# Kernel optimization log

Measured on AMD Instinct MI355X. Metric: run time of the kernel, lower is better.

## Reference

```python
import jax, jax.numpy as jnp
import numpy as np

N_WIRES = 4
N_LAYERS = 3


def _ry_batched(theta):
    # theta: (N,) -> (N,2,2) complex64 RY matrices
    c = jnp.cos(theta / 2).astype(jnp.complex64)
    s = jnp.sin(theta / 2).astype(jnp.complex64)
    row0 = jnp.stack([c, -s], axis=-1)
    row1 = jnp.stack([s, c], axis=-1)
    return jnp.stack([row0, row1], axis=-2)


def _rot(phi, theta, omega):
    # PennyLane Rot(phi,theta,omega) = RZ(omega) @ RY(theta) @ RZ(phi), 2x2 complex
    c = jnp.cos(theta / 2)
    s = jnp.sin(theta / 2)
    m00 = jnp.exp(-0.5j * (phi + omega)) * c
    m01 = -jnp.exp(0.5j * (phi - omega)) * s
    m10 = jnp.exp(-0.5j * (phi - omega)) * s
    m11 = jnp.exp(0.5j * (phi + omega)) * c
    return jnp.stack([jnp.stack([m00, m01]), jnp.stack([m10, m11])]).astype(jnp.complex64)


def _apply_1q(state, U, wire):
    # state: (N,2,2,2,2); U: (2,2) shared or (N,2,2) per-state
    s = jnp.moveaxis(state, wire + 1, 1)
    if U.ndim == 2:
        s = jnp.einsum('ij,njklm->niklm', U, s)
    else:
        s = jnp.einsum('nij,njklm->niklm', U, s)
    return jnp.moveaxis(s, 1, wire + 1)


def _cnot(state, ctrl, tgt):
    # flip target axis where control axis == 1
    s = jnp.moveaxis(state, (ctrl + 1, tgt + 1), (1, 2))
    s = jnp.stack([s[:, 0], jnp.flip(s[:, 1], axis=1)], axis=1)
    return jnp.moveaxis(s, (1, 2), (ctrl + 1, tgt + 1))


def _circuit(angles, params):
    # angles: (N,4) encoding rotations; params: (L,4,3) StronglyEntanglingLayers weights
    N = angles.shape[0]
    state = jnp.zeros((N, 2, 2, 2, 2), jnp.complex64).at[:, 0, 0, 0, 0].set(1.0)
    for w in range(N_WIRES):
        state = _apply_1q(state, _ry_batched(angles[:, w]), w)
    for l in range(params.shape[0]):
        for w in range(N_WIRES):
            state = _apply_1q(state, _rot(params[l, w, 0], params[l, w, 1], params[l, w, 2]), w)
        r = (l % (N_WIRES - 1)) + 1  # PennyLane default ranges
        for w in range(N_WIRES):
            state = _cnot(state, w, (w + r) % N_WIRES)
    probs = state.real ** 2 + state.imag ** 2  # (N,2,2,2,2)
    z = jnp.array([1.0, -1.0], jnp.float32)
    exps = []
    for w in range(N_WIRES):
        axes = tuple(a for a in range(1, 5) if a != w + 1)
        exps.append(probs.sum(axes) @ z)  # <Z_w>
    return jnp.stack(exps, axis=-1)  # (N,4)


def setup_inputs() -> dict:
    key = jax.random.key(0)
    k1, k2, k3, k4 = jax.random.split(key, 4)
    B = 4096
    x = jax.random.uniform(k1, (B, 1, 28, 28), dtype=jnp.float32)
    ansatz_params = jax.random.normal(k2, (N_LAYERS, N_WIRES, 3), dtype=jnp.float32)
    lim = 1.0 / np.sqrt(4.0)
    W = jax.random.uniform(k3, (4, 4), dtype=jnp.float32, minval=-lim, maxval=lim)
    b = jax.random.uniform(k4, (4,), dtype=jnp.float32, minval=-lim, maxval=lim)
    return {'x': x, 'ansatz_params': ansatz_params, 'W': W, 'b': b}


def reference(x, ansatz_params, W, b):
    B = x.shape[0]
    img = x.reshape(B, 28, 28)
    # 2x2 non-overlapping patches, row-major within patch: (B,14,14,2,2)->(B*196,4)
    patches = img.reshape(B, 14, 2, 14, 2).transpose(0, 1, 3, 2, 4).reshape(B * 196, 4)
    feats = _circuit(patches, ansatz_params)  # (B*196,4)
    out = feats @ W.T + b  # per-patch linear
    return out.reshape(B, 196 * 4)
```

## Files before the change

### kernel.cpp

```cpp
#include <hip/hip_runtime.h>
#include <math.h>

#define NW 4
#define NL 3

struct cplx { float re, im; };
__device__ __forceinline__ cplx cmul(cplx a, cplx b){ return {a.re*b.re - a.im*b.im, a.re*b.im + a.im*b.re}; }
__device__ __forceinline__ cplx cadd(cplx a, cplx b){ return {a.re+b.re, a.im+b.im}; }

__global__ void precompute_T(const float* __restrict__ params,
                             const float* __restrict__ W,
                             const float* __restrict__ bias,
                             float* __restrict__ ws)
{
    __shared__ float Ure[16][16], Uim[16][16];
    __shared__ float C[4][16][16];
    const int tid = threadIdx.x;
    const int s = tid >> 4, c = tid & 15;

    Ure[s][c] = (s == c) ? 1.f : 0.f;
    Uim[s][c] = 0.f;
    __syncthreads();

    for (int l = 0; l < NL; ++l) {
        for (int w = 0; w < NW; ++w) {
            float phi = params[(l*NW + w)*3 + 0];
            float th  = params[(l*NW + w)*3 + 1];
            float om  = params[(l*NW + w)*3 + 2];
            float st, ct; sincosf(0.5f*th, &st, &ct);
            float sp, cp; sincosf(-0.5f*(phi+om), &sp, &cp);
            float sm, cm; sincosf(-0.5f*(phi-om), &sm, &cm);
            cplx m00 = {  cp*ct,  sp*ct };
            cplx m01 = { -cm*st,  sm*st };
            cplx m10 = {  cm*st,  sm*st };
            cplx m11 = {  cp*ct, -sp*ct };
            int mask = 1 << (3 - w);
            int b = (s & mask) ? 1 : 0;
            int s0 = s & ~mask, s1 = s | mask;
            cplx g0 = b ? m10 : m00;
            cplx g1 = b ? m11 : m01;
            cplx u0 = { Ure[s0][c], Uim[s0][c] };
            cplx u1 = { Ure[s1][c], Uim[s1][c] };
            cplx nv = cadd(cmul(g0,u0), cmul(g1,u1));
            __syncthreads();
            Ure[s][c] = nv.re; Uim[s][c] = nv.im;
            __syncthreads();
        }
        int r = (l % (NW-1)) + 1;
        for (int w = 0; w < NW; ++w) {
            int ctrl = w, tgt = (w + r) % NW;
            int cmk = 1 << (3 - ctrl), tmk = 1 << (3 - tgt);
            int src = (s & cmk) ? (s ^ tmk) : s;
            float vr = Ure[src][c], vi = Uim[src][c];
            __syncthreads();
            Ure[s][c] = vr; Uim[s][c] = vi;
            __syncthreads();
        }
    }

    {
        float A[4];
        for (int w = 0; w < NW; ++w) {
            int mask = 1 << (3 - w);
            float acc = 0.f;
            for (int rr = 0; rr < 16; ++rr) {
                float zs = (rr & mask) ? -1.f : 1.f;
                acc += zs * (Ure[rr][s]*Ure[rr][c] + Uim[rr][s]*Uim[rr][c]);
            }
            A[w] = acc;
        }
        for (int j = 0; j < 4; ++j) {
            float cj = 0.f;
            for (int w = 0; w < NW; ++w) cj += W[j*4 + w] * A[w];
            C[j][s][c] = cj;
        }
    }
    __syncthreads();

    if (tid < 81) {
        int k = tid;
        int kw[4] = { k/27, (k/9)%3, (k/3)%3, k%3 };
        int sb[4][2], tb[4][2]; float sg[4][2];
        for (int w = 0; w < 4; ++w) {
            int kk = kw[w];
            if (kk == 0)      { sb[w][0]=0; tb[w][0]=0; sg[w][0]= 1.f; sb[w][1]=1; tb[w][1]=1; sg[w][1]= 1.f; }
            else if (kk == 1) { sb[w][0]=0; tb[w][0]=0; sg[w][0]= 1.f; sb[w][1]=1; tb[w][1]=1; sg[w][1]=-1.f; }
            else              { sb[w][0]=0; tb[w][0]=1; sg[w][0]= 1.f; sb[w][1]=1; tb[w][1]=0; sg[w][1]= 1.f; }
        }
        float acc[4] = {0.f,0.f,0.f,0.f};
        for (int m = 0; m < 16; ++m) {
            int ss = 0, tt = 0; float sign = 1.f;
            for (int w = 0; w < 4; ++w) {
                int o = (m >> (3-w)) & 1;
                ss |= sb[w][o] << (3-w);
                tt |= tb[w][o] << (3-w);
                sign *= sg[w][o];
            }
            for (int j = 0; j < 4; ++j) acc[j] += sign * C[j][ss][tt];
        }
        for (int j = 0; j < 4; ++j) {
            float v = acc[j] * (1.f/16.f);
            if (k == 0) v += bias[j];
            ws[k*4 + j] = v;
        }
    }
}

__device__ __forceinline__ void build9(float a0, float a1, float* p) {
    float c0, s0, c1, s1;
    __sincosf(a0, &s0, &c0);
    __sincosf(a1, &s1, &c1);
    p[0] = 1.f;  p[1] = c1;    p[2] = s1;
    p[3] = c0;   p[4] = c0*c1; p[5] = c0*s1;
    p[6] = s0;   p[7] = s0*c1; p[8] = s0*s1;
}

__global__ __launch_bounds__(256) void quanv_main(const float* __restrict__ x,
                                                  const float* __restrict__ T,
                                                  float* __restrict__ out)
{
    __shared__ float4 sT[81];
    const int tid = threadIdx.x;
    if (tid < 81) sT[tid] = ((const float4*)T)[tid];
    __syncthreads();

    int t   = blockIdx.x * 256 + tid;
    int jt  = t % 7;
    int rem = t / 7;
    int i   = rem % 14;
    int b   = rem / 14;

    const float* base = x + b*784 + (2*i)*28 + 4*jt;
    float4 r0 = *(const float4*)(base);
    float4 r1 = *(const float4*)(base + 28);

    float pA01[9], pA23[9], pB01[9], pB23[9];
    build9(r0.x, r0.y, pA01);  build9(r1.x, r1.y, pA23);
    build9(r0.z, r0.w, pB01);  build9(r1.z, r1.w, pB23);

    float oA0=0.f,oA1=0.f,oA2=0.f,oA3=0.f;
    float oB0=0.f,oB1=0.f,oB2=0.f,oB3=0.f;
    #pragma unroll
    for (int u = 0; u < 9; ++u) {
        float au = pA01[u], bu = pB01[u];
        #pragma unroll
        for (int v = 0; v < 9; ++v) {
            float4 tv = sT[u*9 + v];
            float qA = au * pA23[v];
            float qB = bu * pB23[v];
            oA0 = fmaf(tv.x, qA, oA0);  oB0 = fmaf(tv.x, qB, oB0);
            oA1 = fmaf(tv.y, qA, oA1);  oB1 = fmaf(tv.y, qB, oB1);
            oA2 = fmaf(tv.z, qA, oA2);  oB2 = fmaf(tv.z, qB, oB2);
            oA3 = fmaf(tv.w, qA, oA3);  oB3 = fmaf(tv.w, qB, oB3);
        }
    }

    int p = b*196 + i*14 + 2*jt;
    float4* o = (float4*)out + p;
    o[0] = make_float4(oA0, oA1, oA2, oA3);
    o[1] = make_float4(oB0, oB1, oB2, oB3);
}

extern "C" void kernel_launch(void* const* d_in, const int* in_sizes, int n_in,
                              void* d_out, int out_size, void* d_ws, size_t ws_size,
                              hipStream_t stream) {
    const float* x      = (const float*)d_in[0];
    const float* params = (const float*)d_in[1];
    const float* W      = (const float*)d_in[2];
    const float* bias   = (const float*)d_in[3];
    float* out = (float*)d_out;
    float* ws  = (float*)d_ws;

    precompute_T<<<1, 256, 0, stream>>>(params, W, bias, ws);

    const int total  = 4096 * 14 * 7;
    const int blocks = total / 256;
    quanv_main<<<blocks, 256, 0, stream>>>(x, ws, out);
}
```

Before: 84.71 us.

## Process four patches per thread and move unitary build into registers

The main kernel now has each thread handle a 2x2 group of patches (four patches) instead of two. Each shared-memory read of the transfer table is reused across four accumulators, and the block size drops to 64 threads. The precompute kernel builds the 16x16 circuit unitary column by column in registers on 16 threads, replacing the sync-heavy shared-memory gate loop, and computes the gate matrices once. The main risk is higher register pressure and fewer threads in flight in the main kernel.

```diff
diff --git a/kernel.cpp b/kernel.cpp
--- a/kernel.cpp
+++ b/kernel.cpp
@@ -3,75 +3,92 @@
 
 #define NW 4
 #define NL 3
-
-struct cplx { float re, im; };
-__device__ __forceinline__ cplx cmul(cplx a, cplx b){ return {a.re*b.re - a.im*b.im, a.re*b.im + a.im*b.re}; }
-__device__ __forceinline__ cplx cadd(cplx a, cplx b){ return {a.re+b.re, a.im+b.im}; }
 
 __global__ void precompute_T(const float* __restrict__ params,
                              const float* __restrict__ W,
                              const float* __restrict__ bias,
                              float* __restrict__ ws)
 {
+    __shared__ float4 gm4[12][2];
     __shared__ float Ure[16][16], Uim[16][16];
     __shared__ float C[4][16][16];
     const int tid = threadIdx.x;
-    const int s = tid >> 4, c = tid & 15;
-
-    Ure[s][c] = (s == c) ? 1.f : 0.f;
-    Uim[s][c] = 0.f;
-    __syncthreads();
-
-    for (int l = 0; l < NL; ++l) {
-        for (int w = 0; w < NW; ++w) {
-            float phi = params[(l*NW + w)*3 + 0];
-            float th  = params[(l*NW + w)*3 + 1];
-            float om  = params[(l*NW + w)*3 + 2];
-            float st, ct; sincosf(0.5f*th, &st, &ct);
-            float sp, cp; sincosf(-0.5f*(phi+om), &sp, &cp);
-            float sm, cm; sincosf(-0.5f*(phi-om), &sm, &cm);
-            cplx m00 = {  cp*ct,  sp*ct };
-            cplx m01 = { -cm*st,  sm*st };
-            cplx m10 = {  cm*st,  sm*st };
-            cplx m11 = {  cp*ct, -sp*ct };
-            int mask = 1 << (3 - w);
-            int b = (s & mask) ? 1 : 0;
-            int s0 = s & ~mask, s1 = s | mask;
-            cplx g0 = b ? m10 : m00;
-            cplx g1 = b ? m11 : m01;
-            cplx u0 = { Ure[s0][c], Uim[s0][c] };
-            cplx u1 = { Ure[s1][c], Uim[s1][c] };
-            cplx nv = cadd(cmul(g0,u0), cmul(g1,u1));
-            __syncthreads();
-            Ure[s][c] = nv.re; Uim[s][c] = nv.im;
-            __syncthreads();
-        }
-        int r = (l % (NW-1)) + 1;
-        for (int w = 0; w < NW; ++w) {
-            int ctrl = w, tgt = (w + r) % NW;
-            int cmk = 1 << (3 - ctrl), tmk = 1 << (3 - tgt);
-            int src = (s & cmk) ? (s ^ tmk) : s;
-            float vr = Ure[src][c], vi = Uim[src][c];
-            __syncthreads();
-            Ure[s][c] = vr; Uim[s][c] = vi;
-            __syncthreads();
-        }
-    }
+
+    if (tid < 12) {
+        float phi = params[tid*3 + 0];
+        float th  = params[tid*3 + 1];
+        float om  = params[tid*3 + 2];
+        float st, ct; sincosf(0.5f*th, &st, &ct);
+        float sp, cp; sincosf(-0.5f*(phi+om), &sp, &cp);
+        float sm, cm; sincosf(-0.5f*(phi-om), &sm, &cm);
+        gm4[tid][0] = make_float4( cp*ct,  sp*ct, -cm*st,  sm*st);
+        gm4[tid][1] = make_float4( cm*st,  sm*st,  cp*ct, -sp*ct);
+    }
+    __syncthreads();
+
+    if (tid < 16) {
+        const int col = tid;
+        float ur[16], ui[16];
+        #pragma unroll
+        for (int r = 0; r < 16; ++r) { ur[r] = (r == col) ? 1.f : 0.f; ui[r] = 0.f; }
+
+        #pragma unroll
+        for (int l = 0; l < NL; ++l) {
+            #pragma unroll
+            for (int w = 0; w < NW; ++w) {
+                float4 g0 = gm4[l*4 + w][0];
+                float4 g1 = gm4[l*4 + w][1];
+                const int mask = 1 << (3 - w);
+                #pragma unroll
+                for (int s = 0; s < 16; ++s) {
+                    if (s & mask) continue;
+                    const int s1 = s | mask;
+                    float u0r = ur[s],  u0i = ui[s];
+                    float u1r = ur[s1], u1i = ui[s1];
+                    ur[s]  = (g0.x*u0r - g0.y*u0i) + (g0.z*u1r - g0.w*u1i);
+                    ui[s]  = (g0.x*u0i + g0.y*u0r) + (g0.z*u1i + g0.w*u1r);
+                    ur[s1] = (g1.x*u0r - g1.y*u0i) + (g1.z*u1r - g1.w*u1i);
+                    ui[s1] = (g1.x*u0i + g1.y*u0r) + (g1.z*u1i + g1.w*u1r);
+                }
+            }
+            const int rr = (l % (NW-1)) + 1;
+            #pragma unroll
+            for (int w = 0; w < NW; ++w) {
+                const int cmk = 1 << (3 - w);
+                const int tmk = 1 << (3 - ((w + rr) % NW));
+                #pragma unroll
+                for (int s = 0; s < 16; ++s) {
+                    if ((s & cmk) && !(s & tmk)) {
+                        const int s1 = s | tmk;
+                        float tr = ur[s], ti = ui[s];
+                        ur[s] = ur[s1]; ui[s] = ui[s1];
+                        ur[s1] = tr;    ui[s1] = ti;
+                    }
+                }
+            }
+        }
+        #pragma unroll
+        for (int r = 0; r < 16; ++r) { Ure[r][col] = ur[r]; Uim[r][col] = ui[r]; }
+    }
+    __syncthreads();
 
     {
-        float A[4];
-        for (int w = 0; w < NW; ++w) {
-            int mask = 1 << (3 - w);
-            float acc = 0.f;
-            for (int rr = 0; rr < 16; ++rr) {
-                float zs = (rr & mask) ? -1.f : 1.f;
-                acc += zs * (Ure[rr][s]*Ure[rr][c] + Uim[rr][s]*Uim[rr][c]);
-            }
-            A[w] = acc;
-        }
+        const int s = tid >> 4, c = tid & 15;
+        float A0 = 0.f, A1 = 0.f, A2 = 0.f, A3 = 0.f;
+        #pragma unroll
+        for (int r = 0; r < 16; ++r) {
+            float pr = Ure[r][s]*Ure[r][c] + Uim[r][s]*Uim[r][c];
+            A0 += (r & 8) ? -pr : pr;
+            A1 += (r & 4) ? -pr : pr;
+            A2 += (r & 2) ? -pr : pr;
+            A3 += (r & 1) ? -pr : pr;
+        }
+        #pragma unroll
         for (int j = 0; j < 4; ++j) {
-            float cj = 0.f;
-            for (int w = 0; w < NW; ++w) cj += W[j*4 + w] * A[w];
+            float cj = W[j*4+0]*A0;
+            cj += W[j*4+1]*A1;
+            cj += W[j*4+2]*A2;
+            cj += W[j*4+3]*A3;
             C[j][s][c] = cj;
         }
     }
@@ -115,50 +132,66 @@
     p[6] = s0;   p[7] = s0*c1; p[8] = s0*s1;
 }
 
-__global__ __launch_bounds__(256) void quanv_main(const float* __restrict__ x,
-                                                  const float* __restrict__ T,
-                                                  float* __restrict__ out)
+__global__ __launch_bounds__(64, 4) void quanv_main(const float* __restrict__ x,
+                                                    const float* __restrict__ T,
+                                                    float* __restrict__ out)
 {
     __shared__ float4 sT[81];
     const int tid = threadIdx.x;
-    if (tid < 81) sT[tid] = ((const float4*)T)[tid];
-    __syncthreads();
-
-    int t   = blockIdx.x * 256 + tid;
+    sT[tid] = ((const float4*)T)[tid];
+    if (tid < 17) sT[64 + tid] = ((const float4*)T)[64 + tid];
+    __syncthreads();
+
+    int t   = blockIdx.x * 64 + tid;
     int jt  = t % 7;
     int rem = t / 7;
-    int i   = rem % 14;
-    int b   = rem / 14;
-
-    const float* base = x + b*784 + (2*i)*28 + 4*jt;
-    float4 r0 = *(const float4*)(base);
-    float4 r1 = *(const float4*)(base + 28);
+    int i   = rem % 7;
+    int b   = rem / 7;
+
+    const float* base = x + b*784 + (4*i)*28 + 4*jt;
+    float4 q0 = *(const float4*)(base);
+    float4 q1 = *(const float4*)(base + 28);
+    float4 q2 = *(const float4*)(base + 56);
+    float4 q3 = *(const float4*)(base + 84);
 
     float pA01[9], pA23[9], pB01[9], pB23[9];
-    build9(r0.x, r0.y, pA01);  build9(r1.x, r1.y, pA23);
-    build9(r0.z, r0.w, pB01);  build9(r1.z, r1.w, pB23);
+    float pC01[9], pC23[9], pD01[9], pD23[9];
+    build9(q0.x, q0.y, pA01);  build9(q1.x, q1.y, pA23);
+    build9(q0.z, q0.w, pB01);  build9(q1.z, q1.w, pB23);
+    build9(q2.x, q2.y, pC01);  build9(q3.x, q3.y, pC23);
+    build9(q2.z, q2.w, pD01);  build9(q3.z, q3.w, pD23);
 
     float oA0=0.f,oA1=0.f,oA2=0.f,oA3=0.f;
     float oB0=0.f,oB1=0.f,oB2=0.f,oB3=0.f;
+    float oC0=0.f,oC1=0.f,oC2=0.f,oC3=0.f;
+    float oD0=0.f,oD1=0.f,oD2=0.f,oD3=0.f;
     #pragma unroll
     for (int u = 0; u < 9; ++u) {
-        float au = pA01[u], bu = pB01[u];
+        float au = pA01[u], bu = pB01[u], cu = pC01[u], du = pD01[u];
         #pragma unroll
         for (int v = 0; v < 9; ++v) {
             float4 tv = sT[u*9 + v];
             float qA = au * pA23[v];
             float qB = bu * pB23[v];
+            float qC = cu * pC23[v];
+            float qD = du * pD23[v];
             oA0 = fmaf(tv.x, qA, oA0);  oB0 = fmaf(tv.x, qB, oB0);
+            oC0 = fmaf(tv.x, qC, oC0);  oD0 = fmaf(tv.x, qD, oD0);
             oA1 = fmaf(tv.y, qA, oA1);  oB1 = fmaf(tv.y, qB, oB1);
+            oC1 = fmaf(tv.y, qC, oC1);  oD1 = fmaf(tv.y, qD, oD1);
             oA2 = fmaf(tv.z, qA, oA2);  oB2 = fmaf(tv.z, qB, oB2);
+            oC2 = fmaf(tv.z, qC, oC2);  oD2 = fmaf(tv.z, qD, oD2);
             oA3 = fmaf(tv.w, qA, oA3);  oB3 = fmaf(tv.w, qB, oB3);
-        }
-    }
-
-    int p = b*196 + i*14 + 2*jt;
-    float4* o = (float4*)out + p;
-    o[0] = make_float4(oA0, oA1, oA2, oA3);
-    o[1] = make_float4(oB0, oB1, oB2, oB3);
+            oC3 = fmaf(tv.w, qC, oC3);  oD3 = fmaf(tv.w, qD, oD3);
+        }
+    }
+
+    int p = b*196 + (2*i)*14 + 2*jt;
+    float4* o = (float4*)out;
+    o[p]      = make_float4(oA0, oA1, oA2, oA3);
+    o[p + 1]  = make_float4(oB0, oB1, oB2, oB3);
+    o[p + 14] = make_float4(oC0, oC1, oC2, oC3);
+    o[p + 15] = make_float4(oD0, oD1, oD2, oD3);
 }
 
 extern "C" void kernel_launch(void* const* d_in, const int* in_sizes, int n_in,
@@ -173,7 +206,6 @@
 
     precompute_T<<<1, 256, 0, stream>>>(params, W, bias, ws);
 
-    const int total  = 4096 * 14 * 7;
-    const int blocks = total / 256;
-    quanv_main<<<blocks, 256, 0, stream>>>(x, ws, out);
-}
+    const int blocks = (4096 * 7 * 7) / 64;
+    quanv_main<<<blocks, 64, 0, stream>>>(x, ws, out);
+}
```

Result: no change. 84.54 us (-0.2%).
